# Optimization experiments

Hardware: AMD Instinct MI355X
Metric: run time of the kernel (lower is better)

Reference implementation:

```python
import jax, jax.numpy as jnp
import numpy as np

N = 200000
E = 600000
D = 128
EPS = 1e-5


def layer_norm(x, g, b):
    mu = jnp.mean(x, axis=-1, keepdims=True)
    var = jnp.mean(jnp.square(x - mu), axis=-1, keepdims=True)
    return (x - mu) * jax.lax.rsqrt(var + EPS) * g + b


def setup_inputs() -> dict:
    key = jax.random.key(0)
    ks = jax.random.split(key, 8)
    x = jax.random.normal(ks[0], (N, D), dtype=jnp.float32)
    edge_index = jax.random.randint(ks[1], (2, E), 0, N, dtype=jnp.int64)
    lim = 1.0 / np.sqrt(D)
    return {
        "x": x,
        "edge_index": edge_index,
        "ln1_g": jnp.ones((D,), jnp.float32),
        "ln1_b": jnp.zeros((D,), jnp.float32),
        "gcn_w": jax.random.uniform(ks[2], (D, D), jnp.float32, -lim, lim),
        "gcn_b": jnp.zeros((D,), jnp.float32),
        "alpha1": jnp.float32(1e-07),
        "alpha2": jnp.float32(1e-07),
        "ln2_g": jnp.ones((D,), jnp.float32),
        "ln2_b": jnp.zeros((D,), jnp.float32),
        "ff_w": jax.random.uniform(ks[3], (D, D), jnp.float32, -lim, lim),
        "ff_b": jax.random.uniform(ks[4], (D,), jnp.float32, -lim, lim),
    }


def gcn_conv(x, edge_index, W, b):
    # PyG GCNConv: add self-loops, symmetric degree normalization, scatter-add.
    n = x.shape[0]
    loop = jnp.arange(n, dtype=edge_index.dtype)
    src = jnp.concatenate([edge_index[0], loop])  # source j
    dst = jnp.concatenate([edge_index[1], loop])  # target i
    ones = jnp.ones(src.shape[0], dtype=x.dtype)
    deg = jax.ops.segment_sum(ones, dst, num_segments=n)
    dinv = jnp.where(deg > 0, jax.lax.rsqrt(deg), 0.0)
    norm = dinv[src] * dinv[dst]  # [E+N]
    h = x @ W  # [N, D] dense transform first (standard GCN order)
    msg = h[src] * norm[:, None]  # gather + scale
    out = jax.ops.segment_sum(msg, dst, num_segments=n)  # scatter-add
    return out + b


def reference(x, edge_index, ln1_g, ln1_b, gcn_w, gcn_b, alpha1, alpha2,
              ln2_g, ln2_b, ff_w, ff_b):
    h1 = layer_norm(x, ln1_g, ln1_b)
    m = jax.nn.silu(gcn_conv(h1, edge_index, gcn_w, gcn_b))
    x1 = x + alpha1 * m  # res_proj is Identity (in==out)
    h2 = layer_norm(x1, ln2_g, ln2_b)
    f = jax.nn.silu(h2 @ ff_w + ff_b)
    return x1 + alpha2 * f
```

## Files before the change

kernel.cpp:

```cpp
#include <hip/hip_runtime.h>
#include <hip/hip_bf16.h>

#define NN 200000
#define EE 600000
#define DD 128
#define NB 782

typedef __attribute__((ext_vector_type(8))) short short8v;
typedef __attribute__((ext_vector_type(4))) float f32x4;

__device__ __forceinline__ float silu_f(float v) {
    return v * (1.0f / (1.0f + __expf(-v)));
}

__global__ void k_init(int* __restrict__ degi) {
    int i = blockIdx.x * 256 + threadIdx.x;
    if (i < NN) degi[i] = 0;
}

__global__ void k_deg_count(const int* __restrict__ ei, int* __restrict__ degi) {
    int e = blockIdx.x * 256 + threadIdx.x;
    if (e < EE) atomicAdd(&degi[ei[EE + e]], 1);
}

__global__ void k_prep(const float* __restrict__ W, const float* __restrict__ FW,
                       unsigned short* __restrict__ Wt, unsigned short* __restrict__ FWt) {
    const int gid = blockIdx.x * 256 + threadIdx.x;
    const int id = gid & 4095;
    const int col = id >> 5;
    const int kb = (id & 31) * 4;
    const float* src = (gid < 4096) ? W : FW;
    unsigned short* dst = (gid < 4096) ? Wt : FWt;
    unsigned short v[4];
#pragma unroll
    for (int i = 0; i < 4; ++i) {
        __hip_bfloat16 h = __float2bfloat16(src[(size_t)(kb + i) * DD + col]);
        v[i] = *(unsigned short*)&h;
    }
    *(uint2*)&dst[col * DD + kb] = *(uint2*)v;
}

__global__ __launch_bounds__(256) void k_scan1(const int* __restrict__ degi,
                                               int* __restrict__ rs, int* __restrict__ bsum) {
    const int tid = threadIdx.x;
    const int i = blockIdx.x * 256 + tid;
    const int lane = tid & 63, wv = tid >> 6;
    int v = (i < NN) ? degi[i] : 0;
    int x = v;
#pragma unroll
    for (int o = 1; o < 64; o <<= 1) { int y = __shfl_up(x, o); if (lane >= o) x += y; }
    __shared__ int wsum[4];
    if (lane == 63) wsum[wv] = x;
    __syncthreads();
    int off = 0;
    for (int w = 0; w < wv; ++w) off += wsum[w];
    const int incl = x + off;
    if (i < NN) rs[i] = incl - v;
    if (tid == 255) bsum[blockIdx.x] = incl;
}

__global__ void k_scan2(int* __restrict__ bsum) {
    const int lane = threadIdx.x;
    int carry = 0;
    for (int base = 0; base < NB; base += 64) {
        const int i = base + lane;
        int v = (i < NB) ? bsum[i] : 0;
        int x = v;
#pragma unroll
        for (int o = 1; o < 64; o <<= 1) { int y = __shfl_up(x, o); if (lane >= o) x += y; }
        if (i < NB) bsum[i] = x - v + carry;
        carry += __shfl(x, 63);
    }
}

__global__ void k_scan3(int* __restrict__ rs, const int* __restrict__ bsum,
                        int* __restrict__ cursor) {
    const int i = blockIdx.x * 256 + threadIdx.x;
    if (i < NN) {
        const int v = rs[i] + bsum[blockIdx.x];
        rs[i] = v;
        cursor[i] = v;
    }
}

__global__ void k_fill(const int* __restrict__ ei, int* __restrict__ cursor,
                       int* __restrict__ srcs) {
    const int e = blockIdx.x * 256 + threadIdx.x;
    if (e < EE) {
        const int s = ei[e], d = ei[EE + e];
        const int pos = atomicAdd(&cursor[d], 1);
        srcs[pos] = s;
    }
}

__global__ __launch_bounds__(256) void k_ln1_gemm(
    const float* __restrict__ X, const unsigned short* __restrict__ Wt,
    const float* __restrict__ g, const float* __restrict__ b,
    unsigned short* __restrict__ H)
{
    __shared__ __align__(16) char As[128 * 256];

    const int tid = threadIdx.x;
    const int w = tid >> 6, lane = tid & 63;
    const int lm = lane & 15, lg = lane >> 4;
    const int row0 = blockIdx.x * 128;

    short8v bfrag[2][4];
#pragma unroll
    for (int ct = 0; ct < 2; ++ct)
#pragma unroll
        for (int ks = 0; ks < 4; ++ks) {
            const int col = w * 32 + ct * 16 + lm;
            bfrag[ct][ks] = *(const short8v*)((const char*)Wt + col * 256 + ks * 64 + lg * 16);
        }

    const float2 gv = *(const float2*)&g[lane * 2];
    const float2 bv = *(const float2*)&b[lane * 2];
    for (int rr = 0; rr < 32; ++rr) {
        const int r = w * 32 + rr;
        const int grow = row0 + r;
        float2 v = make_float2(0.f, 0.f);
        if (grow < NN) v = *(const float2*)&X[(size_t)grow * DD + lane * 2];
        float s = v.x + v.y, s2 = v.x * v.x + v.y * v.y;
#pragma unroll
        for (int o = 32; o; o >>= 1) { s += __shfl_xor(s, o); s2 += __shfl_xor(s2, o); }
        const float mu = s * (1.f / DD);
        const float rsv = rsqrtf(s2 * (1.f / DD) - mu * mu + 1e-5f);
        __hip_bfloat162 hb;
        hb.x = __float2bfloat16((v.x - mu) * rsv * gv.x + bv.x);
        hb.y = __float2bfloat16((v.y - mu) * rsv * gv.y + bv.y);
        *(unsigned int*)(As + r * 256 + ((lane * 4) ^ ((r & 7) << 4))) = *(unsigned int*)&hb;
    }
    __syncthreads();

    f32x4 acc[8][2];
#pragma unroll
    for (int rt = 0; rt < 8; ++rt) {
        acc[rt][0] = (f32x4){0.f, 0.f, 0.f, 0.f};
        acc[rt][1] = (f32x4){0.f, 0.f, 0.f, 0.f};
    }
#pragma unroll
    for (int ks = 0; ks < 4; ++ks) {
#pragma unroll
        for (int rt = 0; rt < 8; ++rt) {
            const int row = rt * 16 + lm;
            const short8v a = *(const short8v*)(As + row * 256 + ((ks * 64 + lg * 16) ^ ((row & 7) << 4)));
            acc[rt][0] = __builtin_amdgcn_mfma_f32_16x16x32_bf16(a, bfrag[0][ks], acc[rt][0], 0, 0, 0);
            acc[rt][1] = __builtin_amdgcn_mfma_f32_16x16x32_bf16(a, bfrag[1][ks], acc[rt][1], 0, 0, 0);
        }
    }

#pragma unroll
    for (int rt = 0; rt < 8; ++rt)
#pragma unroll
        for (int ct = 0; ct < 2; ++ct)
#pragma unroll
            for (int i = 0; i < 4; ++i) {
                const int grow = row0 + rt * 16 + lg * 4 + i;
                if (grow < NN) {
                    const int col = w * 32 + ct * 16 + lm;
                    __hip_bfloat16 hv = __float2bfloat16(acc[rt][ct][i]);
                    H[(size_t)grow * DD + col] = *(unsigned short*)&hv;
                }
            }
}

__global__ __launch_bounds__(256) void k_gather(
    const int* __restrict__ degi, const int* __restrict__ rs, const int* __restrict__ srcs,
    const unsigned int* __restrict__ Hu,
    const float* __restrict__ X, const float* __restrict__ gcnb,
    const float* __restrict__ a1p,
    float* __restrict__ out,
    float* __restrict__ mu_arr, float* __restrict__ rs_arr)
{
    const int node = blockIdx.x * 4 + (threadIdx.x >> 6);
    const int lane = threadIdx.x & 63;
    if (node >= NN) return;

    const int dcount = degi[node];
    const float degd = 1.0f + (float)dcount;
    const float dinv_d = rsqrtf(degd);

    unsigned int u = Hu[(size_t)node * 64 + lane];
    float2 acc;
    acc.x = __uint_as_float(u << 16) / degd;
    acc.y = __uint_as_float(u & 0xffff0000u) / degd;

    int base = rs[node];
    int remaining = dcount;
    while (remaining > 0) {
        const int cnt = remaining < 64 ? remaining : 64;
        int sp = 0;
        if (lane < cnt) sp = srcs[base + lane];
        int dg = 0;
        if (lane < cnt) dg = degi[sp];
        const float nr = rsqrtf(1.0f + (float)dg) * dinv_d;
        for (int t = 0; t < cnt; ++t) {
            const int s = __shfl(sp, t);
            const float nrm = __shfl(nr, t);
            const unsigned int hu = Hu[(size_t)s * 64 + lane];
            acc.x += __uint_as_float(hu << 16) * nrm;
            acc.y += __uint_as_float(hu & 0xffff0000u) * nrm;
        }
        remaining -= cnt;
        base += cnt;
    }

    const float a1 = *a1p;
    const float2 gb = ((const float2*)gcnb)[lane];
    const float2 xv = ((const float2*)X)[(size_t)node * 64 + lane];
    float2 o;
    o.x = xv.x + a1 * silu_f(acc.x + gb.x);
    o.y = xv.y + a1 * silu_f(acc.y + gb.y);
    ((float2*)out)[(size_t)node * 64 + lane] = o;

    float s = o.x + o.y;
    float s2 = o.x * o.x + o.y * o.y;
    for (int of = 32; of; of >>= 1) { s += __shfl_xor(s, of); s2 += __shfl_xor(s2, of); }
    if (lane == 0) {
        const float mu = s * (1.f / DD);
        const float var = s2 * (1.f / DD) - mu * mu;
        mu_arr[node] = mu;
        rs_arr[node] = rsqrtf(var + 1e-5f);
    }
}

__global__ __launch_bounds__(256) void k_ln2_gemm(
    const unsigned short* __restrict__ FWt,
    const float* __restrict__ g2, const float* __restrict__ b2,
    const float* __restrict__ fb, const float* __restrict__ a2p,
    const float* __restrict__ mu_arr, const float* __restrict__ rs_arr,
    float* __restrict__ out)
{
    __shared__ __align__(16) char As[128 * 256];

    const int tid = threadIdx.x;
    const int w = tid >> 6, lane = tid & 63;
    const int lm = lane & 15, lg = lane >> 4;
    const int row0 = blockIdx.x * 128;

    short8v bfrag[2][4];
#pragma unroll
    for (int ct = 0; ct < 2; ++ct)
#pragma unroll
        for (int ks = 0; ks < 4; ++ks) {
            const int col = w * 32 + ct * 16 + lm;
            bfrag[ct][ks] = *(const short8v*)((const char*)FWt + col * 256 + ks * 64 + lg * 16);
        }
    const float fbv0 = fb[w * 32 + lm];
    const float fbv1 = fb[w * 32 + 16 + lm];

    const float2 gv = *(const float2*)&g2[lane * 2];
    const float2 bv = *(const float2*)&b2[lane * 2];
    for (int rr = 0; rr < 32; ++rr) {
        const int r = w * 32 + rr;
        const int grow = row0 + r;
        float2 v = make_float2(0.f, 0.f);
        float mu = 0.f, rsv = 0.f;
        if (grow < NN) {
            v = *(const float2*)&out[(size_t)grow * DD + lane * 2];
            mu = mu_arr[grow];
            rsv = rs_arr[grow];
        }
        __hip_bfloat162 hb;
        hb.x = __float2bfloat16((v.x - mu) * rsv * gv.x + bv.x);
        hb.y = __float2bfloat16((v.y - mu) * rsv * gv.y + bv.y);
        *(unsigned int*)(As + r * 256 + ((lane * 4) ^ ((r & 7) << 4))) = *(unsigned int*)&hb;
    }
    __syncthreads();

    f32x4 acc[8][2];
#pragma unroll
    for (int rt = 0; rt < 8; ++rt) {
        acc[rt][0] = (f32x4){0.f, 0.f, 0.f, 0.f};
        acc[rt][1] = (f32x4){0.f, 0.f, 0.f, 0.f};
    }
#pragma unroll
    for (int ks = 0; ks < 4; ++ks) {
#pragma unroll
        for (int rt = 0; rt < 8; ++rt) {
            const int row = rt * 16 + lm;
            const short8v a = *(const short8v*)(As + row * 256 + ((ks * 64 + lg * 16) ^ ((row & 7) << 4)));
            acc[rt][0] = __builtin_amdgcn_mfma_f32_16x16x32_bf16(a, bfrag[0][ks], acc[rt][0], 0, 0, 0);
            acc[rt][1] = __builtin_amdgcn_mfma_f32_16x16x32_bf16(a, bfrag[1][ks], acc[rt][1], 0, 0, 0);
        }
    }

    const float a2 = *a2p;
#pragma unroll
    for (int rt = 0; rt < 8; ++rt)
#pragma unroll
        for (int ct = 0; ct < 2; ++ct)
#pragma unroll
            for (int i = 0; i < 4; ++i) {
                const int grow = row0 + rt * 16 + lg * 4 + i;
                if (grow < NN) {
                    const int col = w * 32 + ct * 16 + lm;
                    const float fbc = ct ? fbv1 : fbv0;
                    const size_t idx = (size_t)grow * DD + col;
                    out[idx] = out[idx] + a2 * silu_f(acc[rt][ct][i] + fbc);
                }
            }
}

extern "C" void kernel_launch(void* const* d_in, const int* in_sizes, int n_in,
                              void* d_out, int out_size, void* d_ws, size_t ws_size,
                              hipStream_t stream)
{
    const float* X  = (const float*)d_in[0];
    const int*   EI = (const int*)d_in[1];
    const float* g1 = (const float*)d_in[2];
    const float* b1 = (const float*)d_in[3];
    const float* GW = (const float*)d_in[4];
    const float* gb = (const float*)d_in[5];
    const float* a1 = (const float*)d_in[6];
    const float* a2 = (const float*)d_in[7];
    const float* g2 = (const float*)d_in[8];
    const float* b2 = (const float*)d_in[9];
    const float* FW = (const float*)d_in[10];
    const float* fb = (const float*)d_in[11];
    float* out = (float*)d_out;

    char* ws = (char*)d_ws;
    int*            degi    = (int*)ws;
    unsigned short* H       = (unsigned short*)(ws + 800000);
    int*            rowst   = (int*)(ws + 52000000);
    int*            cursor  = (int*)(ws + 52800000);
    int*            srcs    = (int*)(ws + 53600000);
    int*            bsum    = (int*)(ws + 56000000);
    float*          mu_arr  = (float*)(ws + 56016000);
    float*          rs_arr  = (float*)(ws + 56816000);
    unsigned short* Wt      = (unsigned short*)(ws + 57616000);
    unsigned short* FWt     = (unsigned short*)(ws + 57648768);

    k_init     <<<NB, 256, 0, stream>>>(degi);
    k_deg_count<<<(EE + 255) / 256, 256, 0, stream>>>(EI, degi);
    k_prep     <<<32, 256, 0, stream>>>(GW, FW, Wt, FWt);
    k_ln1_gemm <<<(NN + 127) / 128, 256, 0, stream>>>(X, Wt, g1, b1, H);
    k_scan1    <<<NB, 256, 0, stream>>>(degi, rowst, bsum);
    k_scan2    <<<1, 64, 0, stream>>>(bsum);
    k_scan3    <<<NB, 256, 0, stream>>>(rowst, bsum, cursor);
    k_fill     <<<(EE + 255) / 256, 256, 0, stream>>>(EI, cursor, srcs);
    k_gather   <<<(NN + 3) / 4, 256, 0, stream>>>(degi, rowst, srcs, (const unsigned int*)H,
                                                  X, gb, a1, out, mu_arr, rs_arr);
    k_ln2_gemm <<<(NN + 127) / 128, 256, 0, stream>>>(FWt, g2, b2, fb, a2, mu_arr, rs_arr, out);
}
```

Measured before the change: 509.3 us.

## Prescale H by source dinv and vectorize layernorm row loads

```diff
diff --git a/kernel.cpp b/kernel.cpp
--- a/kernel.cpp
+++ b/kernel.cpp
@@ -11,6 +11,13 @@
 
 __device__ __forceinline__ float silu_f(float v) {
     return v * (1.0f / (1.0f + __expf(-v)));
+}
+
+__device__ __forceinline__ unsigned int pack_bf2(float a, float b) {
+    __hip_bfloat162 hb;
+    hb.x = __float2bfloat16(a);
+    hb.y = __float2bfloat16(b);
+    return *(unsigned int*)&hb;
 }
 
 __global__ void k_init(int* __restrict__ degi) {
@@ -96,13 +103,17 @@
 __global__ __launch_bounds__(256) void k_ln1_gemm(
     const float* __restrict__ X, const unsigned short* __restrict__ Wt,
     const float* __restrict__ g, const float* __restrict__ b,
+    const int* __restrict__ degi,
     unsigned short* __restrict__ H)
 {
     __shared__ __align__(16) char As[128 * 256];
+    __shared__ float dinv_s[128];
 
     const int tid = threadIdx.x;
     const int w = tid >> 6, lane = tid & 63;
     const int lm = lane & 15, lg = lane >> 4;
+    const int sub = lane >> 4;
+    const int lc = lane & 15;
     const int row0 = blockIdx.x * 128;
 
     short8v bfrag[2][4];
@@ -114,22 +125,33 @@
             bfrag[ct][ks] = *(const short8v*)((const char*)Wt + col * 256 + ks * 64 + lg * 16);
         }
 
-    const float2 gv = *(const float2*)&g[lane * 2];
-    const float2 bv = *(const float2*)&b[lane * 2];
-    for (int rr = 0; rr < 32; ++rr) {
-        const int r = w * 32 + rr;
+    const float4 gv0 = *(const float4*)&g[lc * 8];
+    const float4 gv1 = *(const float4*)&g[lc * 8 + 4];
+    const float4 bv0 = *(const float4*)&b[lc * 8];
+    const float4 bv1 = *(const float4*)&b[lc * 8 + 4];
+#pragma unroll
+    for (int it = 0; it < 8; ++it) {
+        const int r = w * 32 + it * 4 + sub;
         const int grow = row0 + r;
-        float2 v = make_float2(0.f, 0.f);
-        if (grow < NN) v = *(const float2*)&X[(size_t)grow * DD + lane * 2];
-        float s = v.x + v.y, s2 = v.x * v.x + v.y * v.y;
-#pragma unroll
-        for (int o = 32; o; o >>= 1) { s += __shfl_xor(s, o); s2 += __shfl_xor(s2, o); }
+        float4 v0 = make_float4(0.f, 0.f, 0.f, 0.f), v1 = v0;
+        if (grow < NN) {
+            v0 = *(const float4*)&X[(size_t)grow * DD + lc * 8];
+            v1 = *(const float4*)&X[(size_t)grow * DD + lc * 8 + 4];
+        }
+        float s = v0.x + v0.y + v0.z + v0.w + v1.x + v1.y + v1.z + v1.w;
+        float s2 = v0.x * v0.x + v0.y * v0.y + v0.z * v0.z + v0.w * v0.w
+                 + v1.x * v1.x + v1.y * v1.y + v1.z * v1.z + v1.w * v1.w;
+#pragma unroll
+        for (int o = 1; o < 16; o <<= 1) { s += __shfl_xor(s, o); s2 += __shfl_xor(s2, o); }
         const float mu = s * (1.f / DD);
         const float rsv = rsqrtf(s2 * (1.f / DD) - mu * mu + 1e-5f);
-        __hip_bfloat162 hb;
-        hb.x = __float2bfloat16((v.x - mu) * rsv * gv.x + bv.x);
-        hb.y = __float2bfloat16((v.y - mu) * rsv * gv.y + bv.y);
-        *(unsigned int*)(As + r * 256 + ((lane * 4) ^ ((r & 7) << 4))) = *(unsigned int*)&hb;
+        uint4 p;
+        p.x = pack_bf2((v0.x - mu) * rsv * gv0.x + bv0.x, (v0.y - mu) * rsv * gv0.y + bv0.y);
+        p.y = pack_bf2((v0.z - mu) * rsv * gv0.z + bv0.z, (v0.w - mu) * rsv * gv0.w + bv0.w);
+        p.z = pack_bf2((v1.x - mu) * rsv * gv1.x + bv1.x, (v1.y - mu) * rsv * gv1.y + bv1.y);
+        p.w = pack_bf2((v1.z - mu) * rsv * gv1.z + bv1.z, (v1.w - mu) * rsv * gv1.w + bv1.w);
+        *(uint4*)(As + r * 256 + ((lc * 16) ^ ((r & 7) << 4))) = p;
+        if (lc == 0 && grow < NN) dinv_s[r] = rsqrtf(1.0f + (float)degi[grow]);
     }
     __syncthreads();
 
@@ -156,10 +178,11 @@
         for (int ct = 0; ct < 2; ++ct)
 #pragma unroll
             for (int i = 0; i < 4; ++i) {
-                const int grow = row0 + rt * 16 + lg * 4 + i;
+                const int lr = rt * 16 + lg * 4 + i;
+                const int grow = row0 + lr;
                 if (grow < NN) {
                     const int col = w * 32 + ct * 16 + lm;
-                    __hip_bfloat16 hv = __float2bfloat16(acc[rt][ct][i]);
+                    __hip_bfloat16 hv = __float2bfloat16(acc[rt][ct][i] * dinv_s[lr]);
                     H[(size_t)grow * DD + col] = *(unsigned short*)&hv;
                 }
             }
@@ -178,13 +201,12 @@
     if (node >= NN) return;
 
     const int dcount = degi[node];
-    const float degd = 1.0f + (float)dcount;
-    const float dinv_d = rsqrtf(degd);
-
-    unsigned int u = Hu[(size_t)node * 64 + lane];
-    float2 acc;
-    acc.x = __uint_as_float(u << 16) / degd;
-    acc.y = __uint_as_float(u & 0xffff0000u) / degd;
+    const float dinv_d = rsqrtf(1.0f + (float)dcount);
+
+    const unsigned int u = Hu[(size_t)node * 64 + lane];
+    float ax = __uint_as_float(u << 16);
+    float ay = __uint_as_float(u & 0xffff0000u);
+    float bx = 0.f, by = 0.f;
 
     int base = rs[node];
     int remaining = dcount;
@@ -192,26 +214,35 @@
         const int cnt = remaining < 64 ? remaining : 64;
         int sp = 0;
         if (lane < cnt) sp = srcs[base + lane];
-        int dg = 0;
-        if (lane < cnt) dg = degi[sp];
-        const float nr = rsqrtf(1.0f + (float)dg) * dinv_d;
-        for (int t = 0; t < cnt; ++t) {
-            const int s = __shfl(sp, t);
-            const float nrm = __shfl(nr, t);
-            const unsigned int hu = Hu[(size_t)s * 64 + lane];
-            acc.x += __uint_as_float(hu << 16) * nrm;
-            acc.y += __uint_as_float(hu & 0xffff0000u) * nrm;
+        int t = 0;
+        for (; t + 1 < cnt; t += 2) {
+            const int s0 = __shfl(sp, t);
+            const int s1 = __shfl(sp, t + 1);
+            const unsigned int u0 = Hu[(size_t)s0 * 64 + lane];
+            const unsigned int u1 = Hu[(size_t)s1 * 64 + lane];
+            ax += __uint_as_float(u0 << 16);
+            ay += __uint_as_float(u0 & 0xffff0000u);
+            bx += __uint_as_float(u1 << 16);
+            by += __uint_as_float(u1 & 0xffff0000u);
+        }
+        if (t < cnt) {
+            const int s0 = __shfl(sp, t);
+            const unsigned int u0 = Hu[(size_t)s0 * 64 + lane];
+            ax += __uint_as_float(u0 << 16);
+            ay += __uint_as_float(u0 & 0xffff0000u);
         }
         remaining -= cnt;
         base += cnt;
     }
+    const float mx = (ax + bx) * dinv_d;
+    const float my = (ay + by) * dinv_d;
 
     const float a1 = *a1p;
     const float2 gb = ((const float2*)gcnb)[lane];
     const float2 xv = ((const float2*)X)[(size_t)node * 64 + lane];
     float2 o;
-    o.x = xv.x + a1 * silu_f(acc.x + gb.x);
-    o.y = xv.y + a1 * silu_f(acc.y + gb.y);
+    o.x = xv.x + a1 * silu_f(mx + gb.x);
+    o.y = xv.y + a1 * silu_f(my + gb.y);
     ((float2*)out)[(size_t)node * 64 + lane] = o;
 
     float s = o.x + o.y;
@@ -237,6 +268,8 @@
     const int tid = threadIdx.x;
     const int w = tid >> 6, lane = tid & 63;
     const int lm = lane & 15, lg = lane >> 4;
+    const int sub = lane >> 4;
+    const int lc = lane & 15;
     const int row0 = blockIdx.x * 128;
 
     short8v bfrag[2][4];
@@ -250,22 +283,28 @@
     const float fbv0 = fb[w * 32 + lm];
     const float fbv1 = fb[w * 32 + 16 + lm];
 
-    const float2 gv = *(const float2*)&g2[lane * 2];
-    const float2 bv = *(const float2*)&b2[lane * 2];
-    for (int rr = 0; rr < 32; ++rr) {
-        const int r = w * 32 + rr;
+    const float4 gv0 = *(const float4*)&g2[lc * 8];
+    const float4 gv1 = *(const float4*)&g2[lc * 8 + 4];
+    const float4 bv0 = *(const float4*)&b2[lc * 8];
+    const float4 bv1 = *(const float4*)&b2[lc * 8 + 4];
+#pragma unroll
+    for (int it = 0; it < 8; ++it) {
+        const int r = w * 32 + it * 4 + sub;
         const int grow = row0 + r;
-        float2 v = make_float2(0.f, 0.f);
+        float4 v0 = make_float4(0.f, 0.f, 0.f, 0.f), v1 = v0;
         float mu = 0.f, rsv = 0.f;
         if (grow < NN) {
-            v = *(const float2*)&out[(size_t)grow * DD + lane * 2];
+            v0 = *(const float4*)&out[(size_t)grow * DD + lc * 8];
+            v1 = *(const float4*)&out[(size_t)grow * DD + lc * 8 + 4];
             mu = mu_arr[grow];
             rsv = rs_arr[grow];
         }
-        __hip_bfloat162 hb;
-        hb.x = __float2bfloat16((v.x - mu) * rsv * gv.x + bv.x);
-        hb.y = __float2bfloat16((v.y - mu) * rsv * gv.y + bv.y);
-        *(unsigned int*)(As + r * 256 + ((lane * 4) ^ ((r & 7) << 4))) = *(unsigned int*)&hb;
+        uint4 p;
+        p.x = pack_bf2((v0.x - mu) * rsv * gv0.x + bv0.x, (v0.y - mu) * rsv * gv0.y + bv0.y);
+        p.y = pack_bf2((v0.z - mu) * rsv * gv0.z + bv0.z, (v0.w - mu) * rsv * gv0.w + bv0.w);
+        p.z = pack_bf2((v1.x - mu) * rsv * gv1.x + bv1.x, (v1.y - mu) * rsv * gv1.y + bv1.y);
+        p.w = pack_bf2((v1.z - mu) * rsv * gv1.z + bv1.z, (v1.w - mu) * rsv * gv1.w + bv1.w);
+        *(uint4*)(As + r * 256 + ((lc * 16) ^ ((r & 7) << 4))) = p;
     }
     __syncthreads();
 
@@ -336,7 +375,7 @@
     k_init     <<<NB, 256, 0, stream>>>(degi);
     k_deg_count<<<(EE + 255) / 256, 256, 0, stream>>>(EI, degi);
     k_prep     <<<32, 256, 0, stream>>>(GW, FW, Wt, FWt);
-    k_ln1_gemm <<<(NN + 127) / 128, 256, 0, stream>>>(X, Wt, g1, b1, H);
+    k_ln1_gemm <<<(NN + 127) / 128, 256, 0, stream>>>(X, Wt, g1, b1, degi, H);
     k_scan1    <<<NB, 256, 0, stream>>>(degi, rowst, bsum);
     k_scan2    <<<1, 64, 0, stream>>>(bsum);
     k_scan3    <<<NB, 256, 0, stream>>>(rowst, bsum, cursor);
```

New measurement: 442.7 us. 1.15x faster.
